# Kernel tuning notes

Measured on AMD Instinct MI355X. Metric: run time of the kernel, lower is better.

Reference implementation:

```python
import jax, jax.numpy as jnp
import numpy as np

D_MODEL = 1024
NHEAD = 16
D_FF = 4096
LN_EPS = 1e-5


def _layer_norm(x, g, b):
    mu = jnp.mean(x, axis=-1, keepdims=True)
    var = jnp.mean(jnp.square(x - mu), axis=-1, keepdims=True)
    return (x - mu) * jax.lax.rsqrt(var + LN_EPS) * g + b


def setup_inputs() -> dict:
    key = jax.random.key(0)
    ks = jax.random.split(key, 12)
    d, f = D_MODEL, D_FF
    s = 1.0 / np.sqrt(d)
    inp = {
        "src": jax.random.normal(ks[0], (2, 2048, d), dtype=jnp.float32),
        "Wq": jax.random.uniform(ks[1], (d, d), jnp.float32, -s, s),
        "bq": jnp.zeros((d,), jnp.float32),
        "Wk": jax.random.uniform(ks[2], (d, d), jnp.float32, -s, s),
        "bk": jnp.zeros((d,), jnp.float32),
        "Wv": jax.random.uniform(ks[3], (d, d), jnp.float32, -s, s),
        "bv": jnp.zeros((d,), jnp.float32),
        "Wo": jax.random.uniform(ks[4], (d, d), jnp.float32, -s, s),
        "bo": jnp.zeros((d,), jnp.float32),
        "W1": jax.random.uniform(ks[5], (d, f), jnp.float32, -s, s),
        "b1": jnp.zeros((f,), jnp.float32),
        "W2": jax.random.uniform(ks[6], (f, d), jnp.float32, -1.0 / np.sqrt(f), 1.0 / np.sqrt(f)),
        "b2": jnp.zeros((d,), jnp.float32),
        "ln1_g": jnp.ones((d,), jnp.float32),
        "ln1_b": jnp.zeros((d,), jnp.float32),
        "ln2_g": jnp.ones((d,), jnp.float32),
        "ln2_b": jnp.zeros((d,), jnp.float32),
    }
    return inp


def reference(src, Wq, bq, Wk, bk, Wv, bv, Wo, bo, W1, b1, W2, b2,
              ln1_g, ln1_b, ln2_g, ln2_b):
    B, S, D = src.shape
    H = NHEAD
    hd = D // H
    # QKV projections, split into heads: [B, H, S, hd]
    q = (src @ Wq + bq).reshape(B, S, H, hd).transpose(0, 2, 1, 3)
    k = (src @ Wk + bk).reshape(B, S, H, hd).transpose(0, 2, 1, 3)
    v = (src @ Wv + bv).reshape(B, S, H, hd).transpose(0, 2, 1, 3)
    # Explicit full-score attention (no mask branch), as in source.
    scores = jnp.einsum("bhqd,bhkd->bhqk", q, k) / jnp.sqrt(jnp.asarray(hd, src.dtype))
    attn = jax.nn.softmax(scores, axis=-1)
    ctx = jnp.einsum("bhqk,bhkd->bhqd", attn, v)
    ctx = ctx.transpose(0, 2, 1, 3).reshape(B, S, D)
    src2 = ctx @ Wo + bo
    x = _layer_norm(src + src2, ln1_g, ln1_b)
    ff = jax.nn.relu(x @ W1 + b1) @ W2 + b2
    out = _layer_norm(x + ff, ln2_g, ln2_b)
    return out
```

## Files before the change

### kernel.cpp

```cpp
#include <hip/hip_runtime.h>
#include <cstdint>
#include <cstddef>

#define SEQ 2048
#define BATCH 2
#define ROWS (BATCH * SEQ)

typedef __attribute__((ext_vector_type(8))) short short8;
typedef __attribute__((ext_vector_type(4))) float f32x4;
typedef __attribute__((ext_vector_type(16))) float f32x16;
typedef __attribute__((ext_vector_type(8))) _Float16 half8;
typedef __attribute__((ext_vector_type(2))) __fp16 fp16x2;

__device__ __forceinline__ unsigned short f2bf(float f) {
  union { float f; uint32_t u; } v; v.f = f;
  uint32_t r = v.u + 0x7fffu + ((v.u >> 16) & 1u);
  return (unsigned short)(r >> 16);
}

__device__ __forceinline__ unsigned short bf2h(unsigned short b) {
  union { uint32_t u; float f; } v; v.u = ((uint32_t)b) << 16;
  union { _Float16 h; unsigned short u; } o; o.h = (_Float16)v.f;
  return o.u;
}

__device__ __forceinline__ void async16(const void* g, void* l) {
  __builtin_amdgcn_global_load_lds((const __attribute__((address_space(1))) void*)g,
                                   (__attribute__((address_space(3))) void*)l, 16, 0, 0);
}

__global__ __launch_bounds__(256) void f2bf_kernel(const float* __restrict__ in,
                                                   unsigned short* __restrict__ out) {
  size_t i = ((size_t)blockIdx.x * 256 + threadIdx.x) * 4;
  float4 vv = *(const float4*)(in + i);
  ushort4 o;
  o.x = f2bf(vv.x); o.y = f2bf(vv.y); o.z = f2bf(vv.z); o.w = f2bf(vv.w);
  *(ushort4*)(out + i) = o;
}

__global__ __launch_bounds__(256) void wtrans(const float* __restrict__ W,
                                              unsigned short* __restrict__ WT,
                                              int K, int N, float scale) {
  __shared__ float t[32][33];
  int n0 = blockIdx.x * 32, k0 = blockIdx.y * 32;
  for (int i = threadIdx.y; i < 32; i += 8)
    t[i][threadIdx.x] = W[(size_t)(k0 + i) * N + n0 + threadIdx.x];
  __syncthreads();
  for (int i = threadIdx.y; i < 32; i += 8)
    WT[(size_t)(n0 + i) * K + k0 + threadIdx.x] = f2bf(t[threadIdx.x][i] * scale);
}

__global__ __launch_bounds__(256) void bias_concat(const float* __restrict__ bq,
                                                   const float* __restrict__ bk,
                                                   const float* __restrict__ bv,
                                                   float* __restrict__ o) {
  int i = blockIdx.x * 256 + threadIdx.x;
  float v = (i < 1024) ? bq[i] * 0.18033688f : (i < 2048 ? bk[i - 1024] : bv[i - 2048]);
  o[i] = v;
}

__global__ __launch_bounds__(256) void vtrans(const unsigned short* __restrict__ qkv,
                                              unsigned short* __restrict__ VT) {
  const int st = blockIdx.x, bh = blockIdx.y, b = bh >> 4, h = bh & 15;
  __shared__ unsigned short t[64][72];
  const int tid = threadIdx.x;
#pragma unroll
  for (int it = 0; it < 2; ++it) {
    int i = it * 256 + tid;
    int s = i >> 3, c = (i & 7) * 8;
    short8 v = *(const short8*)(qkv + ((size_t)b * SEQ + st * 64 + s) * 3072 + 2048 + h * 64 + c);
#pragma unroll
    for (int j = 0; j < 8; ++j) t[c + j][s] = bf2h((unsigned short)v[j]);
  }
  __syncthreads();
#pragma unroll
  for (int it = 0; it < 2; ++it) {
    int i = it * 256 + tid;
    int d = i >> 3, sc = (i & 7) * 8;
    short8 o;
#pragma unroll
    for (int j = 0; j < 8; ++j) o[j] = (short)t[d][sc + j];
    *(short8*)(VT + ((size_t)bh * 64 + d) * 2048 + st * 64 + sc) = o;
  }
}

template <bool RELU>
__global__ __launch_bounds__(512, 2) void gemm_8p(
    const unsigned short* __restrict__ A, const unsigned short* __restrict__ BT,
    const float* __restrict__ bias, unsigned short* __restrict__ outB,
    int M, int N, int K) {
  __shared__ __align__(16) unsigned short lds[65536];
  const int tid = threadIdx.x;
  const int lane = tid & 63, ln = lane & 15, quad = lane >> 4;
  const int wid = tid >> 6, wm = wid >> 2, wn = wid & 3;
  const int m0 = blockIdx.y * 256, n0 = blockIdx.x * 256;
  const int srow = tid >> 2, scol = (tid & 3) * 8;
  const unsigned short* Ag0 = A + (size_t)(m0 + srow) * K + scol;
  const unsigned short* Ag1 = A + (size_t)(m0 + srow + 128) * K + scol;
  const unsigned short* Bg0 = BT + (size_t)(n0 + srow) * K + scol;
  const unsigned short* Bg1 = BT + (size_t)(n0 + srow + 128) * K + scol;
  const int sdst = tid * 8;
  f32x4 acc[8][4] = {};
  short8 fa[2][4];
  short8 fb[2][4];
  const int NT = K >> 6;
#pragma unroll
  for (int kh = 0; kh < 2; ++kh) {
    async16(Ag0 + kh * 32, &lds[kh * 8192 + sdst]);
    async16(Ag1 + kh * 32, &lds[kh * 8192 + sdst + 4096]);
    async16(Bg0 + kh * 32, &lds[16384 + kh * 8192 + sdst]);
    async16(Bg1 + kh * 32, &lds[16384 + kh * 8192 + sdst + 4096]);
  }
  asm volatile("s_waitcnt vmcnt(0)" ::: "memory");
  __builtin_amdgcn_s_barrier();
  {
    const unsigned short* ab = &lds[0];
#pragma unroll
    for (int fi = 0; fi < 4; ++fi)
      fa[1][fi] = *(const short8*)&ab[(wm * 128 + fi * 16 + ln) * 32 + quad * 8];
#pragma unroll
    for (int ni = 0; ni < 4; ++ni)
      fb[0][ni] = *(const short8*)&ab[16384 + (wn * 64 + ni * 16 + ln) * 32 + quad * 8];
  }
  for (int t = 0; t < NT; ++t) {
    const int cb = (t & 1) * 32768, nb = cb ^ 32768;
    const bool more = (t + 1 < NT);
    const int knext = (t + 1) * 64;
#pragma unroll
    for (int p = 0; p < 4; ++p) {
      if (p < 3) {
        const int kk2 = (p + 1) >> 1, mh2 = (p + 1) & 1;
        const unsigned short* ab = &lds[cb + kk2 * 8192];
#pragma unroll
        for (int fi = 0; fi < 4; ++fi)
          fa[p & 1][fi] =
              *(const short8*)&ab[(wm * 128 + mh2 * 64 + fi * 16 + ln) * 32 + quad * 8];
        if (p == 1) {
#pragma unroll
          for (int ni = 0; ni < 4; ++ni)
            fb[1][ni] = *(const short8*)&ab[16384 + (wn * 64 + ni * 16 + ln) * 32 + quad * 8];
        }
      } else if (more) {
        const unsigned short* ab = &lds[nb];
#pragma unroll
        for (int fi = 0; fi < 4; ++fi)
          fa[1][fi] = *(const short8*)&ab[(wm * 128 + fi * 16 + ln) * 32 + quad * 8];
#pragma unroll
        for (int ni = 0; ni < 4; ++ni)
          fb[0][ni] = *(const short8*)&ab[16384 + (wn * 64 + ni * 16 + ln) * 32 + quad * 8];
      }
      if (more && p < 2) {
        unsigned short* d = &lds[nb + p * 8192];
        async16(Ag0 + knext + p * 32, d + sdst);
        async16(Ag1 + knext + p * 32, d + sdst + 4096);
        async16(Bg0 + knext + p * 32, d + 16384 + sdst);
        async16(Bg1 + knext + p * 32, d + 16384 + sdst + 4096);
      }
      if (p == 0) {
        if (more) asm volatile("s_waitcnt vmcnt(4)" ::: "memory");
        else      asm volatile("s_waitcnt vmcnt(0)" ::: "memory");
      } else if (p == 2 && more) {
        asm volatile("s_waitcnt vmcnt(4)" ::: "memory");
      }
      __builtin_amdgcn_s_barrier();
      __builtin_amdgcn_s_setprio(1);
#pragma unroll
      for (int fi = 0; fi < 4; ++fi)
#pragma unroll
        for (int ni = 0; ni < 4; ++ni)
          acc[(p & 1) * 4 + fi][ni] = __builtin_amdgcn_mfma_f32_16x16x32_bf16(
              fa[(p + 1) & 1][fi], fb[p >> 1][ni], acc[(p & 1) * 4 + fi][ni], 0, 0, 0);
      __builtin_amdgcn_s_setprio(0);
      if (p < 3 || more) __builtin_amdgcn_s_barrier();
    }
  }
#pragma unroll
  for (int mi = 0; mi < 8; ++mi)
#pragma unroll
    for (int ni = 0; ni < 4; ++ni)
#pragma unroll
      for (int reg = 0; reg < 4; ++reg) {
        int row = m0 + wm * 128 + mi * 16 + quad * 4 + reg;
        int col = n0 + wn * 64 + ni * 16 + ln;
        float v = acc[mi][ni][reg] + bias[col];
        if (RELU) v = fmaxf(v, 0.f);
        outB[(size_t)row * N + col] = f2bf(v);
      }
}

template <bool RELU, bool OUTBF, bool HASRES>
__global__ __launch_bounds__(256) void gemm_bt64(
    const unsigned short* __restrict__ A, const unsigned short* __restrict__ BT,
    const float* __restrict__ bias, const float* __restrict__ Rres,
    float* __restrict__ outF, unsigned short* __restrict__ outB,
    int M, int N, int K) {
  __shared__ unsigned short As[4][128 * 32];
  __shared__ unsigned short Bs[4][64 * 32];
  const int tid = threadIdx.x;
  const int lane = tid & 63, ln = lane & 15, quad = lane >> 4;
  const int w = tid >> 6;
  const int m0 = blockIdx.y * 128, n0 = blockIdx.x * 64;
  const int mw = w * 32;
  f32x4 acc[2][4] = {};
  const int i0 = tid, i1 = tid + 256;
  const int r0 = i0 >> 2, kc0 = (i0 & 3) * 8;
  const int r1 = i1 >> 2, kc1 = (i1 & 3) * 8;
  for (int k0 = 0; k0 < K; k0 += 128) {
    __syncthreads();
#pragma unroll
    for (int p = 0; p < 4; ++p) {
      const int kp = k0 + p * 32;
      async16(A + (size_t)(m0 + r0) * K + kp + kc0, &As[p][i0 * 8]);
      async16(A + (size_t)(m0 + r1) * K + kp + kc1, &As[p][i1 * 8]);
      async16(BT + (size_t)(n0 + r0) * K + kp + kc0, &Bs[p][i0 * 8]);
    }
    __syncthreads();
#pragma unroll
    for (int p = 0; p < 4; ++p) {
      short8 a[2], b[4];
#pragma unroll
      for (int mi = 0; mi < 2; ++mi)
        a[mi] = *(const short8*)&As[p][(mw + mi * 16 + ln) * 32 + quad * 8];
#pragma unroll
      for (int ni = 0; ni < 4; ++ni)
        b[ni] = *(const short8*)&Bs[p][(ni * 16 + ln) * 32 + quad * 8];
#pragma unroll
      for (int mi = 0; mi < 2; ++mi)
#pragma unroll
        for (int ni = 0; ni < 4; ++ni)
          acc[mi][ni] = __builtin_amdgcn_mfma_f32_16x16x32_bf16(a[mi], b[ni], acc[mi][ni], 0, 0, 0);
    }
  }
#pragma unroll
  for (int mi = 0; mi < 2; ++mi) {
#pragma unroll
    for (int ni = 0; ni < 4; ++ni) {
#pragma unroll
      for (int reg = 0; reg < 4; ++reg) {
        int row = m0 + mw + mi * 16 + quad * 4 + reg;
        int col = n0 + ni * 16 + ln;
        float v = acc[mi][ni][reg] + bias[col];
        if (HASRES) v += Rres[(size_t)row * N + col];
        if (RELU) v = fmaxf(v, 0.f);
        if (OUTBF) outB[(size_t)row * N + col] = f2bf(v);
        else outF[(size_t)row * N + col] = v;
      }
    }
  }
}

__global__ __launch_bounds__(128, 2) void attn_kernel(const unsigned short* __restrict__ qkv,
                                                      const unsigned short* __restrict__ VT,
                                                      unsigned short* __restrict__ ctx) {
  const int qt = blockIdx.x;
  const int bh = blockIdx.y, b = bh >> 4, h = bh & 15;
  const int tid = threadIdx.x;
  const int w = tid >> 6, lane = tid & 63;
  const int r32 = lane & 31, hi = lane >> 5, r7 = r32 & 7;
  __shared__ __align__(16) unsigned short Ks[2 * 4096];
  __shared__ __align__(16) unsigned short Vs[2 * 4096];
  const size_t rowbase = (size_t)b * SEQ;
  const unsigned short* kbase = qkv + rowbase * 3072 + 1024 + h * 64;
  const unsigned short* vbase = VT + (size_t)bh * 64 * 2048;
  int r_[4], s_[4], wsw_[4];
#pragma unroll
  for (int i = 0; i < 4; ++i) {
    int idx = i * 128 + tid;
    r_[i] = idx >> 3; s_[i] = idx & 7;
    wsw_[i] = r_[i] * 64 + ((s_[i] ^ (r_[i] & 7)) * 8);
  }
  short8 qf[4];
  {
    const unsigned short* qp = qkv + (rowbase + qt * 64 + w * 32 + r32) * 3072 + h * 64;
#pragma unroll
    for (int dc = 0; dc < 4; ++dc) qf[dc] = *(const short8*)(qp + dc * 16 + hi * 8);
  }
  short8 kst[4], vst[4];
#pragma unroll
  for (int i = 0; i < 4; ++i) {
    kst[i] = *(const short8*)(kbase + (size_t)r_[i] * 3072 + s_[i] * 8);
    vst[i] = *(const short8*)(vbase + (size_t)r_[i] * 2048 + s_[i] * 8);
  }
#pragma unroll
  for (int i = 0; i < 4; ++i) {
    *(short8*)&Ks[wsw_[i]] = kst[i];
    *(short8*)&Vs[wsw_[i]] = vst[i];
  }
  __syncthreads();
  f32x16 oacc0 = {}, oacc1 = {};
  float lsum = 0.f;
  int cur = 0;
  for (int kt = 0; kt < 32; ++kt) {
    if (kt < 31) {
      const unsigned short* kp = kbase + (size_t)(kt + 1) * 64 * 3072;
      const unsigned short* vp = vbase + (kt + 1) * 64;
#pragma unroll
      for (int i = 0; i < 4; ++i) {
        kst[i] = *(const short8*)(kp + (size_t)r_[i] * 3072 + s_[i] * 8);
        vst[i] = *(const short8*)(vp + (size_t)r_[i] * 2048 + s_[i] * 8);
      }
    }
    const unsigned short* Kb = &Ks[cur];
    const unsigned short* Vb = &Vs[cur];
    f32x16 z0 = {}, z1 = {};
    __builtin_amdgcn_s_setprio(1);
#pragma unroll
    for (int dc = 0; dc < 4; ++dc) {
      const int sl = ((dc * 2 + hi) ^ r7) * 8;
      short8 kf0 = *(const short8*)&Kb[r32 * 64 + sl];
      short8 kf1 = *(const short8*)&Kb[(32 + r32) * 64 + sl];
      z0 = __builtin_amdgcn_mfma_f32_32x32x16_bf16(kf0, qf[dc], z0, 0, 0, 0);
      z1 = __builtin_amdgcn_mfma_f32_32x32x16_bf16(kf1, qf[dc], z1, 0, 0, 0);
    }
    __builtin_amdgcn_s_setprio(0);
    half8 pf[4];
#pragma unroll
    for (int kc = 0; kc < 4; ++kc) {
      float e[8];
#pragma unroll
      for (int j = 0; j < 8; ++j) {
        float zz = (kc < 2) ? z0[(kc & 1) * 8 + j] : z1[(kc & 1) * 8 + j];
        e[j] = __builtin_amdgcn_exp2f(zz);
        lsum += e[j];
      }
      union { fp16x2 hh; unsigned int u; } a0, a1, b0, b1;
      a0.hh = __builtin_amdgcn_cvt_pkrtz(e[0], e[1]);
      a1.hh = __builtin_amdgcn_cvt_pkrtz(e[2], e[3]);
      b0.hh = __builtin_amdgcn_cvt_pkrtz(e[4], e[5]);
      b1.hh = __builtin_amdgcn_cvt_pkrtz(e[6], e[7]);
      asm volatile("v_permlane32_swap_b32 %0, %1" : "+v"(a0.u), "+v"(b0.u));
      asm volatile("v_permlane32_swap_b32 %0, %1" : "+v"(a1.u), "+v"(b1.u));
      union { unsigned int u[4]; half8 hh; } fr;
      fr.u[0] = a0.u; fr.u[1] = a1.u; fr.u[2] = b0.u; fr.u[3] = b1.u;
      pf[kc] = fr.hh;
    }
    __builtin_amdgcn_s_setprio(1);
#pragma unroll
    for (int kc = 0; kc < 4; ++kc) {
      const int sl = ((kc * 2 + hi) ^ r7) * 8;
      half8 vf0 = *(const half8*)&Vb[r32 * 64 + sl];
      half8 vf1 = *(const half8*)&Vb[(32 + r32) * 64 + sl];
      oacc0 = __builtin_amdgcn_mfma_f32_32x32x16_f16(vf0, pf[kc], oacc0, 0, 0, 0);
      oacc1 = __builtin_amdgcn_mfma_f32_32x32x16_f16(vf1, pf[kc], oacc1, 0, 0, 0);
    }
    __builtin_amdgcn_s_setprio(0);
    if (kt < 31) {
      const int nb = cur ^ 4096;
#pragma unroll
      for (int i = 0; i < 4; ++i) {
        *(short8*)&Ks[nb + wsw_[i]] = kst[i];
        *(short8*)&Vs[nb + wsw_[i]] = vst[i];
      }
      __syncthreads();
      cur = nb;
    }
  }
  float tot = lsum + __shfl_xor(lsum, 32);
  float rl = 1.0f / tot;
  const size_t orow = (rowbase + (size_t)qt * 64 + w * 32 + r32) * 1024 + h * 64 + hi * 4;
#pragma unroll
  for (int tq = 0; tq < 4; ++tq) {
    ushort4 o0, o1;
    o0.x = f2bf(oacc0[tq * 4 + 0] * rl); o0.y = f2bf(oacc0[tq * 4 + 1] * rl);
    o0.z = f2bf(oacc0[tq * 4 + 2] * rl); o0.w = f2bf(oacc0[tq * 4 + 3] * rl);
    *(ushort4*)(ctx + orow + tq * 8) = o0;
    o1.x = f2bf(oacc1[tq * 4 + 0] * rl); o1.y = f2bf(oacc1[tq * 4 + 1] * rl);
    o1.z = f2bf(oacc1[tq * 4 + 2] * rl); o1.w = f2bf(oacc1[tq * 4 + 3] * rl);
    *(ushort4*)(ctx + orow + 32 + tq * 8) = o1;
  }
}

__global__ __launch_bounds__(256) void ln_kernel(const float* __restrict__ y,
                                                 const float* __restrict__ g,
                                                 const float* __restrict__ bb,
                                                 float* __restrict__ outF,
                                                 unsigned short* __restrict__ outB) {
  const int row = blockIdx.x;
  const int tid = threadIdx.x;
  const float* yr = y + (size_t)row * 1024;
  float v[4]; float s = 0.f, s2 = 0.f;
#pragma unroll
  for (int j = 0; j < 4; ++j) {
    v[j] = yr[tid + j * 256];
    s += v[j]; s2 += v[j] * v[j];
  }
#pragma unroll
  for (int off = 1; off < 64; off <<= 1) {
    s += __shfl_xor(s, off);
    s2 += __shfl_xor(s2, off);
  }
  __shared__ float ws1[4], ws2[4];
  if ((tid & 63) == 0) { ws1[tid >> 6] = s; ws2[tid >> 6] = s2; }
  __syncthreads();
  s = ws1[0] + ws1[1] + ws1[2] + ws1[3];
  s2 = ws2[0] + ws2[1] + ws2[2] + ws2[3];
  const float mu = s * (1.f / 1024.f);
  const float var = s2 * (1.f / 1024.f) - mu * mu;
  const float rstd = rsqrtf(var + 1e-5f);
#pragma unroll
  for (int j = 0; j < 4; ++j) {
    int c = tid + j * 256;
    float val = (v[j] - mu) * rstd * g[c] + bb[c];
    if (outF) outF[(size_t)row * 1024 + c] = val;
    if (outB) outB[(size_t)row * 1024 + c] = f2bf(val);
  }
}

extern "C" void kernel_launch(void* const* d_in, const int* in_sizes, int n_in,
                              void* d_out, int out_size, void* d_ws, size_t ws_size,
                              hipStream_t stream) {
  const float* src = (const float*)d_in[0];
  const float* Wq = (const float*)d_in[1];
  const float* bq = (const float*)d_in[2];
  const float* Wk = (const float*)d_in[3];
  const float* bk = (const float*)d_in[4];
  const float* Wv = (const float*)d_in[5];
  const float* bv = (const float*)d_in[6];
  const float* Wo = (const float*)d_in[7];
  const float* bo = (const float*)d_in[8];
  const float* W1 = (const float*)d_in[9];
  const float* b1 = (const float*)d_in[10];
  const float* W2 = (const float*)d_in[11];
  const float* b2 = (const float*)d_in[12];
  const float* ln1g = (const float*)d_in[13];
  const float* ln1b = (const float*)d_in[14];
  const float* ln2g = (const float*)d_in[15];
  const float* ln2b = (const float*)d_in[16];
  float* out = (float*)d_out;

  char* ws = (char*)d_ws;
  unsigned short* qkvT = (unsigned short*)(ws + 0);
  unsigned short* WoT  = (unsigned short*)(ws + 6291456);
  unsigned short* W1T  = (unsigned short*)(ws + 8388608);
  unsigned short* W2T  = (unsigned short*)(ws + 16777216);
  float*          biasq = (float*)(ws + 25165824);
  unsigned short* xbf  = (unsigned short*)(ws + 25178112);
  unsigned short* qkv  = (unsigned short*)(ws + 33566720);
  unsigned short* hbuf = qkv;
  unsigned short* ctx  = (unsigned short*)(ws + 58732544);
  float*          ybuf = (float*)(ws + 67121152);
  unsigned short* VT   = (unsigned short*)(ws + 67121152);
  float*          xf   = (float*)(ws + 83898368);

  const float QSCALE = 0.18033688f;

  f2bf_kernel<<<4096, 256, 0, stream>>>(src, xbf);
  wtrans<<<dim3(32, 32), dim3(32, 8), 0, stream>>>(Wq, qkvT, 1024, 1024, QSCALE);
  wtrans<<<dim3(32, 32), dim3(32, 8), 0, stream>>>(Wk, qkvT + 1024 * 1024, 1024, 1024, 1.0f);
  wtrans<<<dim3(32, 32), dim3(32, 8), 0, stream>>>(Wv, qkvT + 2048 * 1024, 1024, 1024, 1.0f);
  wtrans<<<dim3(32, 32), dim3(32, 8), 0, stream>>>(Wo, WoT, 1024, 1024, 1.0f);
  wtrans<<<dim3(128, 32), dim3(32, 8), 0, stream>>>(W1, W1T, 1024, 4096, 1.0f);
  wtrans<<<dim3(32, 128), dim3(32, 8), 0, stream>>>(W2, W2T, 4096, 1024, 1.0f);
  bias_concat<<<12, 256, 0, stream>>>(bq, bk, bv, biasq);

  gemm_8p<false><<<dim3(12, 16), 512, 0, stream>>>(xbf, qkvT, biasq, qkv, ROWS, 3072, 1024);
  vtrans<<<dim3(32, 32), 256, 0, stream>>>(qkv, VT);
  attn_kernel<<<dim3(32, 32), 128, 0, stream>>>(qkv, VT, ctx);
  gemm_bt64<false, false, true><<<dim3(16, 32), 256, 0, stream>>>(
      ctx, WoT, bo, src, ybuf, nullptr, ROWS, 1024, 1024);
  ln_kernel<<<4096, 256, 0, stream>>>(ybuf, ln1g, ln1b, xf, xbf);
  gemm_8p<true><<<dim3(16, 16), 512, 0, stream>>>(xbf, W1T, b1, hbuf, ROWS, 4096, 1024);
  gemm_bt64<false, false, true><<<dim3(16, 32), 256, 0, stream>>>(
      hbuf, W2T, b2, xf, ybuf, nullptr, ROWS, 1024, 4096);
  ln_kernel<<<4096, 256, 0, stream>>>(ybuf, ln2g, ln2b, out, nullptr);
}
```

Before: 373.8 us.

## Load K/V attention fragments directly from global into registers, drop LDS staging

Result: slower. 456.7 us (+22.2%).

```diff
diff --git a/kernel.cpp b/kernel.cpp
--- a/kernel.cpp
+++ b/kernel.cpp
@@ -256,63 +256,50 @@
   const int bh = blockIdx.y, b = bh >> 4, h = bh & 15;
   const int tid = threadIdx.x;
   const int w = tid >> 6, lane = tid & 63;
-  const int r32 = lane & 31, hi = lane >> 5, r7 = r32 & 7;
-  __shared__ __align__(16) unsigned short Ks[2 * 4096];
-  __shared__ __align__(16) unsigned short Vs[2 * 4096];
+  const int r32 = lane & 31, hi = lane >> 5;
   const size_t rowbase = (size_t)b * SEQ;
-  const unsigned short* kbase = qkv + rowbase * 3072 + 1024 + h * 64;
-  const unsigned short* vbase = VT + (size_t)bh * 64 * 2048;
-  int r_[4], s_[4], wsw_[4];
-#pragma unroll
-  for (int i = 0; i < 4; ++i) {
-    int idx = i * 128 + tid;
-    r_[i] = idx >> 3; s_[i] = idx & 7;
-    wsw_[i] = r_[i] * 64 + ((s_[i] ^ (r_[i] & 7)) * 8);
-  }
   short8 qf[4];
   {
     const unsigned short* qp = qkv + (rowbase + qt * 64 + w * 32 + r32) * 3072 + h * 64;
 #pragma unroll
     for (int dc = 0; dc < 4; ++dc) qf[dc] = *(const short8*)(qp + dc * 16 + hi * 8);
   }
-  short8 kst[4], vst[4];
-#pragma unroll
-  for (int i = 0; i < 4; ++i) {
-    kst[i] = *(const short8*)(kbase + (size_t)r_[i] * 3072 + s_[i] * 8);
-    vst[i] = *(const short8*)(vbase + (size_t)r_[i] * 2048 + s_[i] * 8);
-  }
-#pragma unroll
-  for (int i = 0; i < 4; ++i) {
-    *(short8*)&Ks[wsw_[i]] = kst[i];
-    *(short8*)&Vs[wsw_[i]] = vst[i];
-  }
-  __syncthreads();
+  const unsigned short* kp0 = qkv + (rowbase + r32) * 3072 + 1024 + h * 64 + hi * 8;
+  const unsigned short* kp1 = kp0 + (size_t)32 * 3072;
+  const unsigned short* vp0 = VT + ((size_t)bh * 64 + r32) * 2048 + hi * 8;
+  const unsigned short* vp1 = vp0 + (size_t)32 * 2048;
+  short8 kreg[8];
+  half8 vreg[8];
+#pragma unroll
+  for (int dc = 0; dc < 4; ++dc) {
+    kreg[dc] = *(const short8*)(kp0 + dc * 16);
+    kreg[4 + dc] = *(const short8*)(kp1 + dc * 16);
+  }
+#pragma unroll
+  for (int kc = 0; kc < 4; ++kc) {
+    vreg[kc] = *(const half8*)(vp0 + kc * 16);
+    vreg[4 + kc] = *(const half8*)(vp1 + kc * 16);
+  }
   f32x16 oacc0 = {}, oacc1 = {};
   float lsum = 0.f;
-  int cur = 0;
   for (int kt = 0; kt < 32; ++kt) {
-    if (kt < 31) {
-      const unsigned short* kp = kbase + (size_t)(kt + 1) * 64 * 3072;
-      const unsigned short* vp = vbase + (kt + 1) * 64;
-#pragma unroll
-      for (int i = 0; i < 4; ++i) {
-        kst[i] = *(const short8*)(kp + (size_t)r_[i] * 3072 + s_[i] * 8);
-        vst[i] = *(const short8*)(vp + (size_t)r_[i] * 2048 + s_[i] * 8);
-      }
-    }
-    const unsigned short* Kb = &Ks[cur];
-    const unsigned short* Vb = &Vs[cur];
     f32x16 z0 = {}, z1 = {};
     __builtin_amdgcn_s_setprio(1);
 #pragma unroll
     for (int dc = 0; dc < 4; ++dc) {
-      const int sl = ((dc * 2 + hi) ^ r7) * 8;
-      short8 kf0 = *(const short8*)&Kb[r32 * 64 + sl];
-      short8 kf1 = *(const short8*)&Kb[(32 + r32) * 64 + sl];
-      z0 = __builtin_amdgcn_mfma_f32_32x32x16_bf16(kf0, qf[dc], z0, 0, 0, 0);
-      z1 = __builtin_amdgcn_mfma_f32_32x32x16_bf16(kf1, qf[dc], z1, 0, 0, 0);
+      z0 = __builtin_amdgcn_mfma_f32_32x32x16_bf16(kreg[dc], qf[dc], z0, 0, 0, 0);
+      z1 = __builtin_amdgcn_mfma_f32_32x32x16_bf16(kreg[4 + dc], qf[dc], z1, 0, 0, 0);
     }
     __builtin_amdgcn_s_setprio(0);
+    if (kt < 31) {
+      const unsigned short* nk0 = kp0 + (size_t)(kt + 1) * 64 * 3072;
+      const unsigned short* nk1 = nk0 + (size_t)32 * 3072;
+#pragma unroll
+      for (int dc = 0; dc < 4; ++dc) {
+        kreg[dc] = *(const short8*)(nk0 + dc * 16);
+        kreg[4 + dc] = *(const short8*)(nk1 + dc * 16);
+      }
+    }
     half8 pf[4];
 #pragma unroll
     for (int kc = 0; kc < 4; ++kc) {
@@ -337,22 +324,18 @@
     __builtin_amdgcn_s_setprio(1);
 #pragma unroll
     for (int kc = 0; kc < 4; ++kc) {
-      const int sl = ((kc * 2 + hi) ^ r7) * 8;
-      half8 vf0 = *(const half8*)&Vb[r32 * 64 + sl];
-      half8 vf1 = *(const half8*)&Vb[(32 + r32) * 64 + sl];
-      oacc0 = __builtin_amdgcn_mfma_f32_32x32x16_f16(vf0, pf[kc], oacc0, 0, 0, 0);
-      oacc1 = __builtin_amdgcn_mfma_f32_32x32x16_f16(vf1, pf[kc], oacc1, 0, 0, 0);
+      oacc0 = __builtin_amdgcn_mfma_f32_32x32x16_f16(vreg[kc], pf[kc], oacc0, 0, 0, 0);
+      oacc1 = __builtin_amdgcn_mfma_f32_32x32x16_f16(vreg[4 + kc], pf[kc], oacc1, 0, 0, 0);
     }
     __builtin_amdgcn_s_setprio(0);
     if (kt < 31) {
-      const int nb = cur ^ 4096;
-#pragma unroll
-      for (int i = 0; i < 4; ++i) {
-        *(short8*)&Ks[nb + wsw_[i]] = kst[i];
-        *(short8*)&Vs[nb + wsw_[i]] = vst[i];
-      }
-      __syncthreads();
-      cur = nb;
+      const unsigned short* nv0 = vp0 + (kt + 1) * 64;
+      const unsigned short* nv1 = vp1 + (kt + 1) * 64;
+#pragma unroll
+      for (int kc = 0; kc < 4; ++kc) {
+        vreg[kc] = *(const half8*)(nv0 + kc * 16);
+        vreg[4 + kc] = *(const half8*)(nv1 + kc * 16);
+      }
     }
   }
   float tot = lsum + __shfl_xor(lsum, 32);
```

## Split-K the FFN down-projection with 256x256 tiles and fuse reduction into LayerNorm

Applied to the files above, without the earlier changes.

Measured after the change: 384.3 us. 2.8% more time.

```diff
diff --git a/kernel.cpp b/kernel.cpp
--- a/kernel.cpp
+++ b/kernel.cpp
@@ -188,6 +188,117 @@
       }
 }
 
+__global__ __launch_bounds__(512, 2) void gemm_8p_sk(
+    const unsigned short* __restrict__ A, const unsigned short* __restrict__ BT,
+    float* __restrict__ p0lo, float* __restrict__ p0hi,
+    float* __restrict__ p1lo, float* __restrict__ p1hi,
+    float* __restrict__ p2lo, float* __restrict__ p2hi,
+    float* __restrict__ p3lo, float* __restrict__ p3hi,
+    int M, int N, int K, int KH) {
+  __shared__ __align__(16) unsigned short lds[65536];
+  const int tid = threadIdx.x;
+  const int lane = tid & 63, ln = lane & 15, quad = lane >> 4;
+  const int wid = tid >> 6, wm = wid >> 2, wn = wid & 3;
+  const int m0 = blockIdx.y * 256, n0 = blockIdx.x * 256;
+  const int kbeg = blockIdx.z * KH;
+  float *Plo, *Phi;
+  if (blockIdx.z == 0)      { Plo = p0lo; Phi = p0hi; }
+  else if (blockIdx.z == 1) { Plo = p1lo; Phi = p1hi; }
+  else if (blockIdx.z == 2) { Plo = p2lo; Phi = p2hi; }
+  else                      { Plo = p3lo; Phi = p3hi; }
+  const int srow = tid >> 2, scol = (tid & 3) * 8;
+  const unsigned short* Ag0 = A + (size_t)(m0 + srow) * K + kbeg + scol;
+  const unsigned short* Ag1 = A + (size_t)(m0 + srow + 128) * K + kbeg + scol;
+  const unsigned short* Bg0 = BT + (size_t)(n0 + srow) * K + kbeg + scol;
+  const unsigned short* Bg1 = BT + (size_t)(n0 + srow + 128) * K + kbeg + scol;
+  const int sdst = tid * 8;
+  f32x4 acc[8][4] = {};
+  short8 fa[2][4];
+  short8 fb[2][4];
+  const int NT = KH >> 6;
+#pragma unroll
+  for (int kh = 0; kh < 2; ++kh) {
+    async16(Ag0 + kh * 32, &lds[kh * 8192 + sdst]);
+    async16(Ag1 + kh * 32, &lds[kh * 8192 + sdst + 4096]);
+    async16(Bg0 + kh * 32, &lds[16384 + kh * 8192 + sdst]);
+    async16(Bg1 + kh * 32, &lds[16384 + kh * 8192 + sdst + 4096]);
+  }
+  asm volatile("s_waitcnt vmcnt(0)" ::: "memory");
+  __builtin_amdgcn_s_barrier();
+  {
+    const unsigned short* ab = &lds[0];
+#pragma unroll
+    for (int fi = 0; fi < 4; ++fi)
+      fa[1][fi] = *(const short8*)&ab[(wm * 128 + fi * 16 + ln) * 32 + quad * 8];
+#pragma unroll
+    for (int ni = 0; ni < 4; ++ni)
+      fb[0][ni] = *(const short8*)&ab[16384 + (wn * 64 + ni * 16 + ln) * 32 + quad * 8];
+  }
+  for (int t = 0; t < NT; ++t) {
+    const int cb = (t & 1) * 32768, nb = cb ^ 32768;
+    const bool more = (t + 1 < NT);
+    const int knext = (t + 1) * 64;
+#pragma unroll
+    for (int p = 0; p < 4; ++p) {
+      if (p < 3) {
+        const int kk2 = (p + 1) >> 1, mh2 = (p + 1) & 1;
+        const unsigned short* ab = &lds[cb + kk2 * 8192];
+#pragma unroll
+        for (int fi = 0; fi < 4; ++fi)
+          fa[p & 1][fi] =
+              *(const short8*)&ab[(wm * 128 + mh2 * 64 + fi * 16 + ln) * 32 + quad * 8];
+        if (p == 1) {
+#pragma unroll
+          for (int ni = 0; ni < 4; ++ni)
+            fb[1][ni] = *(const short8*)&ab[16384 + (wn * 64 + ni * 16 + ln) * 32 + quad * 8];
+        }
+      } else if (more) {
+        const unsigned short* ab = &lds[nb];
+#pragma unroll
+        for (int fi = 0; fi < 4; ++fi)
+          fa[1][fi] = *(const short8*)&ab[(wm * 128 + fi * 16 + ln) * 32 + quad * 8];
+#pragma unroll
+        for (int ni = 0; ni < 4; ++ni)
+          fb[0][ni] = *(const short8*)&ab[16384 + (wn * 64 + ni * 16 + ln) * 32 + quad * 8];
+      }
+      if (more && p < 2) {
+        unsigned short* d = &lds[nb + p * 8192];
+        async16(Ag0 + knext + p * 32, d + sdst);
+        async16(Ag1 + knext + p * 32, d + sdst + 4096);
+        async16(Bg0 + knext + p * 32, d + 16384 + sdst);
+        async16(Bg1 + knext + p * 32, d + 16384 + sdst + 4096);
+      }
+      if (p == 0) {
+        if (more) asm volatile("s_waitcnt vmcnt(4)" ::: "memory");
+        else      asm volatile("s_waitcnt vmcnt(0)" ::: "memory");
+      } else if (p == 2 && more) {
+        asm volatile("s_waitcnt vmcnt(4)" ::: "memory");
+      }
+      __builtin_amdgcn_s_barrier();
+      __builtin_amdgcn_s_setprio(1);
+#pragma unroll
+      for (int fi = 0; fi < 4; ++fi)
+#pragma unroll
+        for (int ni = 0; ni < 4; ++ni)
+          acc[(p & 1) * 4 + fi][ni] = __builtin_amdgcn_mfma_f32_16x16x32_bf16(
+              fa[(p + 1) & 1][fi], fb[p >> 1][ni], acc[(p & 1) * 4 + fi][ni], 0, 0, 0);
+      __builtin_amdgcn_s_setprio(0);
+      if (p < 3 || more) __builtin_amdgcn_s_barrier();
+    }
+  }
+#pragma unroll
+  for (int mi = 0; mi < 8; ++mi)
+#pragma unroll
+    for (int ni = 0; ni < 4; ++ni)
+#pragma unroll
+      for (int reg = 0; reg < 4; ++reg) {
+        int row = m0 + wm * 128 + mi * 16 + quad * 4 + reg;
+        int col = n0 + wn * 64 + ni * 16 + ln;
+        float* P = (row < 2048) ? Plo : Phi;
+        P[(size_t)(row & 2047) * N + col] = acc[mi][ni][reg];
+      }
+}
+
 template <bool RELU, bool OUTBF, bool HASRES>
 __global__ __launch_bounds__(256) void gemm_bt64(
     const unsigned short* __restrict__ A, const unsigned short* __restrict__ BT,
@@ -257,6 +368,7 @@
   const int tid = threadIdx.x;
   const int w = tid >> 6, lane = tid & 63;
   const int r32 = lane & 31, hi = lane >> 5, r7 = r32 & 7;
+  const int sw2 = (r32 >> 3) & 3;
   __shared__ __align__(16) unsigned short Ks[2 * 4096];
   __shared__ __align__(16) unsigned short Vs[2 * 4096];
   const size_t rowbase = (size_t)b * SEQ;
@@ -267,7 +379,7 @@
   for (int i = 0; i < 4; ++i) {
     int idx = i * 128 + tid;
     r_[i] = idx >> 3; s_[i] = idx & 7;
-    wsw_[i] = r_[i] * 64 + ((s_[i] ^ (r_[i] & 7)) * 8);
+    wsw_[i] = r_[i] * 64 + ((s_[i] ^ (r_[i] & 7) ^ ((r_[i] >> 3) & 3)) * 8);
   }
   short8 qf[4];
   {
@@ -306,7 +418,7 @@
     __builtin_amdgcn_s_setprio(1);
 #pragma unroll
     for (int dc = 0; dc < 4; ++dc) {
-      const int sl = ((dc * 2 + hi) ^ r7) * 8;
+      const int sl = (((dc * 2 + hi) ^ r7 ^ sw2) & 7) * 8;
       short8 kf0 = *(const short8*)&Kb[r32 * 64 + sl];
       short8 kf1 = *(const short8*)&Kb[(32 + r32) * 64 + sl];
       z0 = __builtin_amdgcn_mfma_f32_32x32x16_bf16(kf0, qf[dc], z0, 0, 0, 0);
@@ -337,7 +449,7 @@
     __builtin_amdgcn_s_setprio(1);
 #pragma unroll
     for (int kc = 0; kc < 4; ++kc) {
-      const int sl = ((kc * 2 + hi) ^ r7) * 8;
+      const int sl = (((kc * 2 + hi) ^ r7 ^ sw2) & 7) * 8;
       half8 vf0 = *(const half8*)&Vb[r32 * 64 + sl];
       half8 vf1 = *(const half8*)&Vb[(32 + r32) * 64 + sl];
       oacc0 = __builtin_amdgcn_mfma_f32_32x32x16_f16(vf0, pf[kc], oacc0, 0, 0, 0);
@@ -403,6 +515,50 @@
     float val = (v[j] - mu) * rstd * g[c] + bb[c];
     if (outF) outF[(size_t)row * 1024 + c] = val;
     if (outB) outB[(size_t)row * 1024 + c] = f2bf(val);
+  }
+}
+
+__global__ __launch_bounds__(256) void ln_red_kernel(
+    const float* __restrict__ p0lo, const float* __restrict__ p0hi,
+    const float* __restrict__ p1lo, const float* __restrict__ p1hi,
+    const float* __restrict__ p2lo, const float* __restrict__ p2hi,
+    const float* __restrict__ p3lo, const float* __restrict__ p3hi,
+    const float* __restrict__ bias, const float* __restrict__ res,
+    const float* __restrict__ g, const float* __restrict__ bb,
+    float* __restrict__ outF) {
+  const int row = blockIdx.x;
+  const int tid = threadIdx.x;
+  const size_t rb = (size_t)row * 1024;
+  const size_t rbl = (size_t)(row & 2047) * 1024;
+  const bool lo = (row < 2048);
+  const float* q0 = (lo ? p0lo : p0hi) + rbl;
+  const float* q1 = (lo ? p1lo : p1hi) + rbl;
+  const float* q2 = (lo ? p2lo : p2hi) + rbl;
+  const float* q3 = (lo ? p3lo : p3hi) + rbl;
+  float v[4]; float s = 0.f, s2 = 0.f;
+#pragma unroll
+  for (int j = 0; j < 4; ++j) {
+    int c = tid + j * 256;
+    v[j] = (q0[c] + q1[c]) + (q2[c] + q3[c]) + bias[c] + res[rb + c];
+    s += v[j]; s2 += v[j] * v[j];
+  }
+#pragma unroll
+  for (int off = 1; off < 64; off <<= 1) {
+    s += __shfl_xor(s, off);
+    s2 += __shfl_xor(s2, off);
+  }
+  __shared__ float ws1[4], ws2[4];
+  if ((tid & 63) == 0) { ws1[tid >> 6] = s; ws2[tid >> 6] = s2; }
+  __syncthreads();
+  s = ws1[0] + ws1[1] + ws1[2] + ws1[3];
+  s2 = ws2[0] + ws2[1] + ws2[2] + ws2[3];
+  const float mu = s * (1.f / 1024.f);
+  const float var = s2 * (1.f / 1024.f) - mu * mu;
+  const float rstd = rsqrtf(var + 1e-5f);
+#pragma unroll
+  for (int j = 0; j < 4; ++j) {
+    int c = tid + j * 256;
+    outF[rb + c] = (v[j] - mu) * rstd * g[c] + bb[c];
   }
 }
 
@@ -442,6 +598,11 @@
   unsigned short* VT   = (unsigned short*)(ws + 67121152);
   float*          xf   = (float*)(ws + 83898368);
 
+  float* P0lo = ybuf;              float* P0hi = ybuf + (size_t)2048 * 1024;
+  float* P1lo = (float*)(ws + 0);  float* P1hi = P1lo + (size_t)2048 * 1024;
+  float* P2lo = (float*)ctx;       float* P2hi = (float*)xbf;
+  float* P3lo = out;               float* P3hi = out + (size_t)2048 * 1024;
+
   const float QSCALE = 0.18033688f;
 
   f2bf_kernel<<<4096, 256, 0, stream>>>(src, xbf);
@@ -460,7 +621,8 @@
       ctx, WoT, bo, src, ybuf, nullptr, ROWS, 1024, 1024);
   ln_kernel<<<4096, 256, 0, stream>>>(ybuf, ln1g, ln1b, xf, xbf);
   gemm_8p<true><<<dim3(16, 16), 512, 0, stream>>>(xbf, W1T, b1, hbuf, ROWS, 4096, 1024);
-  gemm_bt64<false, false, true><<<dim3(16, 32), 256, 0, stream>>>(
-      hbuf, W2T, b2, xf, ybuf, nullptr, ROWS, 1024, 4096);
-  ln_kernel<<<4096, 256, 0, stream>>>(ybuf, ln2g, ln2b, out, nullptr);
-}
+  gemm_8p_sk<<<dim3(4, 16, 4), 512, 0, stream>>>(
+      hbuf, W2T, P0lo, P0hi, P1lo, P1hi, P2lo, P2hi, P3lo, P3hi, ROWS, 1024, 4096, 1024);
+  ln_red_kernel<<<4096, 256, 0, stream>>>(
+      P0lo, P0hi, P1lo, P1hi, P2lo, P2hi, P3lo, P3hi, b2, xf, ln2g, ln2b, out);
+}
```

## Software-pipeline QK^T one tile ahead of softmax/PV in attention kernel

Applied to the files above, without the earlier changes.

Result: no change. 374.9 us (+0.3%).

```diff
diff --git a/kernel.cpp b/kernel.cpp
--- a/kernel.cpp
+++ b/kernel.cpp
@@ -257,6 +257,7 @@
   const int tid = threadIdx.x;
   const int w = tid >> 6, lane = tid & 63;
   const int r32 = lane & 31, hi = lane >> 5, r7 = r32 & 7;
+  const int sw2 = (r32 >> 3) & 3;
   __shared__ __align__(16) unsigned short Ks[2 * 4096];
   __shared__ __align__(16) unsigned short Vs[2 * 4096];
   const size_t rowbase = (size_t)b * SEQ;
@@ -267,7 +268,7 @@
   for (int i = 0; i < 4; ++i) {
     int idx = i * 128 + tid;
     r_[i] = idx >> 3; s_[i] = idx & 7;
-    wsw_[i] = r_[i] * 64 + ((s_[i] ^ (r_[i] & 7)) * 8);
+    wsw_[i] = r_[i] * 64 + ((s_[i] ^ (r_[i] & 7) ^ ((r_[i] >> 3) & 3)) * 8);
   }
   short8 qf[4];
   {
@@ -277,49 +278,76 @@
   }
   short8 kst[4], vst[4];
 #pragma unroll
-  for (int i = 0; i < 4; ++i) {
+  for (int i = 0; i < 4; ++i)
     kst[i] = *(const short8*)(kbase + (size_t)r_[i] * 3072 + s_[i] * 8);
-    vst[i] = *(const short8*)(vbase + (size_t)r_[i] * 2048 + s_[i] * 8);
-  }
-#pragma unroll
-  for (int i = 0; i < 4; ++i) {
-    *(short8*)&Ks[wsw_[i]] = kst[i];
-    *(short8*)&Vs[wsw_[i]] = vst[i];
-  }
+#pragma unroll
+  for (int i = 0; i < 4; ++i) *(short8*)&Ks[4096 + wsw_[i]] = kst[i];
   __syncthreads();
+  f32x16 zA0 = {}, zA1 = {}, zB0 = {}, zB1 = {};
+  {
+    const unsigned short* kp1g = kbase + (size_t)64 * 3072;
+#pragma unroll
+    for (int i = 0; i < 4; ++i) {
+      kst[i] = *(const short8*)(kp1g + (size_t)r_[i] * 3072 + s_[i] * 8);
+      vst[i] = *(const short8*)(vbase + (size_t)r_[i] * 2048 + s_[i] * 8);
+    }
+    const unsigned short* Kb = &Ks[4096];
+    __builtin_amdgcn_s_setprio(1);
+#pragma unroll
+    for (int dc = 0; dc < 4; ++dc) {
+      const int sl = (((dc * 2 + hi) ^ r7 ^ sw2) & 7) * 8;
+      short8 kf0 = *(const short8*)&Kb[r32 * 64 + sl];
+      short8 kf1 = *(const short8*)&Kb[(32 + r32) * 64 + sl];
+      zA0 = __builtin_amdgcn_mfma_f32_32x32x16_bf16(kf0, qf[dc], zA0, 0, 0, 0);
+      zA1 = __builtin_amdgcn_mfma_f32_32x32x16_bf16(kf1, qf[dc], zA1, 0, 0, 0);
+    }
+    __builtin_amdgcn_s_setprio(0);
+#pragma unroll
+    for (int i = 0; i < 4; ++i) {
+      *(short8*)&Ks[wsw_[i]] = kst[i];
+      *(short8*)&Vs[wsw_[i]] = vst[i];
+    }
+    __syncthreads();
+  }
+  int cur = 0;
   f32x16 oacc0 = {}, oacc1 = {};
   float lsum = 0.f;
-  int cur = 0;
-  for (int kt = 0; kt < 32; ++kt) {
+  auto iter = [&](int kt, f32x16& zc0, f32x16& zc1, f32x16& zn0, f32x16& zn1) {
+    if (kt < 30) {
+      const unsigned short* kp = kbase + (size_t)(kt + 2) * 64 * 3072;
+#pragma unroll
+      for (int i = 0; i < 4; ++i)
+        kst[i] = *(const short8*)(kp + (size_t)r_[i] * 3072 + s_[i] * 8);
+    }
     if (kt < 31) {
-      const unsigned short* kp = kbase + (size_t)(kt + 1) * 64 * 3072;
       const unsigned short* vp = vbase + (kt + 1) * 64;
 #pragma unroll
-      for (int i = 0; i < 4; ++i) {
-        kst[i] = *(const short8*)(kp + (size_t)r_[i] * 3072 + s_[i] * 8);
+      for (int i = 0; i < 4; ++i)
         vst[i] = *(const short8*)(vp + (size_t)r_[i] * 2048 + s_[i] * 8);
-      }
     }
     const unsigned short* Kb = &Ks[cur];
     const unsigned short* Vb = &Vs[cur];
-    f32x16 z0 = {}, z1 = {};
-    __builtin_amdgcn_s_setprio(1);
-#pragma unroll
-    for (int dc = 0; dc < 4; ++dc) {
-      const int sl = ((dc * 2 + hi) ^ r7) * 8;
-      short8 kf0 = *(const short8*)&Kb[r32 * 64 + sl];
-      short8 kf1 = *(const short8*)&Kb[(32 + r32) * 64 + sl];
-      z0 = __builtin_amdgcn_mfma_f32_32x32x16_bf16(kf0, qf[dc], z0, 0, 0, 0);
-      z1 = __builtin_amdgcn_mfma_f32_32x32x16_bf16(kf1, qf[dc], z1, 0, 0, 0);
-    }
-    __builtin_amdgcn_s_setprio(0);
+    if (kt < 31) {
+      f32x16 t0 = {}, t1 = {};
+      __builtin_amdgcn_s_setprio(1);
+#pragma unroll
+      for (int dc = 0; dc < 4; ++dc) {
+        const int sl = (((dc * 2 + hi) ^ r7 ^ sw2) & 7) * 8;
+        short8 kf0 = *(const short8*)&Kb[r32 * 64 + sl];
+        short8 kf1 = *(const short8*)&Kb[(32 + r32) * 64 + sl];
+        t0 = __builtin_amdgcn_mfma_f32_32x32x16_bf16(kf0, qf[dc], t0, 0, 0, 0);
+        t1 = __builtin_amdgcn_mfma_f32_32x32x16_bf16(kf1, qf[dc], t1, 0, 0, 0);
+      }
+      __builtin_amdgcn_s_setprio(0);
+      zn0 = t0; zn1 = t1;
+    }
     half8 pf[4];
 #pragma unroll
     for (int kc = 0; kc < 4; ++kc) {
       float e[8];
 #pragma unroll
       for (int j = 0; j < 8; ++j) {
-        float zz = (kc < 2) ? z0[(kc & 1) * 8 + j] : z1[(kc & 1) * 8 + j];
+        float zz = (kc < 2) ? zc0[(kc & 1) * 8 + j] : zc1[(kc & 1) * 8 + j];
         e[j] = __builtin_amdgcn_exp2f(zz);
         lsum += e[j];
       }
@@ -337,7 +365,7 @@
     __builtin_amdgcn_s_setprio(1);
 #pragma unroll
     for (int kc = 0; kc < 4; ++kc) {
-      const int sl = ((kc * 2 + hi) ^ r7) * 8;
+      const int sl = (((kc * 2 + hi) ^ r7 ^ sw2) & 7) * 8;
       half8 vf0 = *(const half8*)&Vb[r32 * 64 + sl];
       half8 vf1 = *(const half8*)&Vb[(32 + r32) * 64 + sl];
       oacc0 = __builtin_amdgcn_mfma_f32_32x32x16_f16(vf0, pf[kc], oacc0, 0, 0, 0);
@@ -346,14 +374,19 @@
     __builtin_amdgcn_s_setprio(0);
     if (kt < 31) {
       const int nb = cur ^ 4096;
-#pragma unroll
-      for (int i = 0; i < 4; ++i) {
-        *(short8*)&Ks[nb + wsw_[i]] = kst[i];
-        *(short8*)&Vs[nb + wsw_[i]] = vst[i];
-      }
+      if (kt < 30) {
+#pragma unroll
+        for (int i = 0; i < 4; ++i) *(short8*)&Ks[nb + wsw_[i]] = kst[i];
+      }
+#pragma unroll
+      for (int i = 0; i < 4; ++i) *(short8*)&Vs[nb + wsw_[i]] = vst[i];
       __syncthreads();
       cur = nb;
     }
+  };
+  for (int kt = 0; kt < 32; kt += 2) {
+    iter(kt, zA0, zA1, zB0, zB1);
+    iter(kt + 1, zB0, zB1, zA0, zA1);
   }
   float tot = lsum + __shfl_xor(lsum, 32);
   float rl = 1.0f / tot;
```
